# Optimization experiments

Hardware: AMD Instinct MI355X
Metric: run time of the kernel (lower is better)

The kernel has to match this reference:

```python
import jax, jax.numpy as jnp
import numpy as np

INPUT_DIM = 64
LATENT_DIM = 128
B, N = 16, 8192
SQRT3 = float(np.sqrt(3.0))
SQRT5 = float(np.sqrt(5.0))
PATH_COEFF = float(1.0 / np.sqrt(INPUT_DIM))  # e3nn 'element' path norm, w3j(0,l,l)=I/sqrt(2l+1)


def _spherical_harmonics_lmax2(pos):
    """e3nn o3.spherical_harmonics(lmax=2, normalize=True, normalization='component').
    Returns (sh0 [..],  sh1 [..,3], sh2 [..,5])."""
    n = pos * jax.lax.rsqrt(jnp.sum(pos * pos, axis=-1, keepdims=True))
    x, y, z = n[..., 0], n[..., 1], n[..., 2]
    sh0 = jnp.ones_like(x)
    sh1 = SQRT3 * n  # component norm: sqrt(3) * unit vector, order (x,y,z)
    # l=2 block (component norm = sqrt(5) * norm-normalized polynomials)
    sh2 = SQRT5 * jnp.stack([
        SQRT3 * x * z,
        SQRT3 * x * y,
        y * y - 0.5 * (x * x + z * z),
        SQRT3 * y * z,
        (SQRT3 / 2.0) * (z * z - x * x),
    ], axis=-1)
    return sh0, sh1, sh2


def setup_inputs() -> dict:
    key = jax.random.key(0)
    k1, k2, k3, k4 = jax.random.split(key, 4)
    features = jax.random.normal(k1, (B, N, INPUT_DIM), dtype=jnp.float32)
    pos = jax.random.normal(k2, (B, N, 3), dtype=jnp.float32)
    # e3nn FullyConnectedTensorProduct weights ~ N(0,1); one [u,w] matrix per path
    W0 = jax.random.normal(k3, (INPUT_DIM, LATENT_DIM), dtype=jnp.float32)  # 0e x 0e -> 0e
    W1 = jax.random.normal(k4, (INPUT_DIM, LATENT_DIM), dtype=jnp.float32)  # 0e x 1o -> 1o
    return {"features": features, "pos": pos, "W0": W0, "W1": W1}


def reference(features, pos, W0, W1):
    sh0, sh1, sh2 = _spherical_harmonics_lmax2(pos)  # sh2 has no output path (dropped)
    # scalar path: out[b,n,w] = coeff * sum_u feat[b,n,u] W0[u,w] * sh0
    scalars = PATH_COEFF * jnp.einsum('bnu,uw->bnw', features, W0) * sh0[..., None]
    # vector path: out[b,n,w,k] = coeff * (feat @ W1)[b,n,w] * sh1[b,n,k]
    vec = PATH_COEFF * jnp.einsum('bnu,uw->bnw', features, W1)
    vectors = vec[..., :, None] * sh1[..., None, :]  # [B,N,LATENT,3]
    latent = jnp.concatenate(
        [scalars, vectors.reshape(*vectors.shape[:-2], LATENT_DIM * 3)], axis=-1
    )  # [B, N, LATENT + 3*LATENT]
    return jnp.mean(latent, axis=1)  # [B, 4*LATENT]
```

## Files before the change

### kernel.cpp

```cpp
#include <hip/hip_runtime.h>

#define B_ 16
#define N_ 8192
#define U_ 64
#define W_ 128
#define BLOCKS_PER_B 32
#define ROWS_PER_BLOCK (N_ / BLOCKS_PER_B)
#define GRID_ (B_ * BLOCKS_PER_B)

typedef float f32x4 __attribute__((ext_vector_type(4)));


__global__ __launch_bounds__(256, 2) void so3_reduce_kernel(
    const float* __restrict__ feat,
    const float* __restrict__ pos,
    float* __restrict__ ws)
{
    const int blk   = blockIdx.x;
    const int b     = blk / BLOCKS_PER_B;
    const int chunk = blk % BLOCKS_PER_B;
    const int row0  = chunk * ROWS_PER_BLOCK;
    const int tid   = threadIdx.x;
    const int grp   = tid & 15;
    const int rsub  = tid >> 4;

    __shared__ f32x4 nlds[ROWS_PER_BLOCK];
    {
        const float* p = pos + ((size_t)b * N_ + row0 + tid) * 3;
        const float px = p[0], py = p[1], pz = p[2];
        const float inv = rsqrtf(px * px + py * py + pz * pz);
        f32x4 v;
        v.x = px * inv; v.y = py * inv; v.z = pz * inv; v.w = 1.0f;
        nlds[tid] = v;
    }
    __syncthreads();

    const f32x4* fbase = (const f32x4*)(feat + (size_t)b * N_ * U_);

    f32x4 fb[16];
    #pragma unroll
    for (int it = 0; it < 16; ++it) {
        const int nl = it * 16 + rsub;
        fb[it] = __builtin_nontemporal_load(
            &fbase[(size_t)(row0 + nl) * 16 + grp]);
    }

    float acc[4][4] = {{0.f,0.f,0.f,0.f},{0.f,0.f,0.f,0.f},
                       {0.f,0.f,0.f,0.f},{0.f,0.f,0.f,0.f}};

    #pragma unroll
    for (int it = 0; it < 16; ++it) {
        const int nl = it * 16 + rsub;
        const f32x4 f  = fb[it];
        const f32x4 nv = nlds[nl];
        #pragma unroll
        for (int k = 0; k < 4; ++k) {
            const float nk = (k == 0) ? nv.x : (k == 1) ? nv.y
                           : (k == 2) ? nv.z : nv.w;
            acc[0][k] = fmaf(f.x, nk, acc[0][k]);
            acc[1][k] = fmaf(f.y, nk, acc[1][k]);
            acc[2][k] = fmaf(f.z, nk, acc[2][k]);
            acc[3][k] = fmaf(f.w, nk, acc[3][k]);
        }
    }

    __shared__ float lds[256][17];
    #pragma unroll
    for (int i = 0; i < 4; ++i) {
        lds[tid][i * 4 + 0] = acc[i][0];
        lds[tid][i * 4 + 1] = acc[i][1];
        lds[tid][i * 4 + 2] = acc[i][2];
        lds[tid][i * 4 + 3] = acc[i][3];
    }
    __syncthreads();

    const int u    = tid >> 2;
    const int j    = tid & 3;
    const int ug   = u >> 2;
    const int sub  = u & 3;
    const int slot = (j == 0) ? (sub * 4 + 3) : (sub * 4 + (j - 1));
    float s = 0.f;
    #pragma unroll
    for (int src = 0; src < 16; ++src) {
        const int t = (src & 3) * 64 + (src >> 2) * 16 + ug;
        s += lds[t][slot];
    }
    ws[(size_t)blk * 256 + tid] = s;
}

__global__ __launch_bounds__(512) void so3_finalize_kernel(
    const float* __restrict__ ws,
    const float* __restrict__ W0,
    const float* __restrict__ W1,
    float* __restrict__ out)
{
    const int b   = blockIdx.x;
    const int tid = threadIdx.x;

    const int u4   = tid & 63;
    const int cgrp = tid >> 6;

    __shared__ float4 smf4[8][64];
    __shared__ float  sm[256];

    {
        const float4* base = (const float4*)(ws + (size_t)b * BLOCKS_PER_B * 256);
        float4 a = {0.f, 0.f, 0.f, 0.f};
        #pragma unroll
        for (int c = 0; c < 4; ++c) {
            const float4 v = base[(size_t)(cgrp * 4 + c) * 64 + u4];
            a.x += v.x; a.y += v.y; a.z += v.z; a.w += v.w;
        }
        smf4[cgrp][u4] = a;
    }
    __syncthreads();

    if (tid < 64) {
        float4 t = smf4[0][tid];
        #pragma unroll
        for (int g = 1; g < 8; ++g) {
            const float4 v = smf4[g][tid];
            t.x += v.x; t.y += v.y; t.z += v.z; t.w += v.w;
        }
        ((float4*)sm)[tid] = t;
    }
    __syncthreads();

    const float scaleS = 0.125f / (float)N_;
    const float scaleV = 0.125f * 1.7320508075688772f / (float)N_;

    const int o = tid;
    float acc = 0.f;
    if (o < 128) {
        #pragma unroll
        for (int uu = 0; uu < 64; ++uu) acc += sm[uu * 4] * W0[uu * 128 + o];
        out[b * 512 + o] = acc * scaleS;
    } else {
        const int idx = o - 128;
        const int w = idx / 3;
        const int k = idx - 3 * w;
        #pragma unroll
        for (int uu = 0; uu < 64; ++uu) acc += sm[uu * 4 + 1 + k] * W1[uu * 128 + w];
        out[b * 512 + 128 + idx] = acc * scaleV;
    }
}

extern "C" void kernel_launch(void* const* d_in, const int* in_sizes, int n_in,
                              void* d_out, int out_size, void* d_ws, size_t ws_size,
                              hipStream_t stream) {
    const float* feat = (const float*)d_in[0];
    const float* pos  = (const float*)d_in[1];
    const float* W0   = (const float*)d_in[2];
    const float* W1   = (const float*)d_in[3];
    float* out = (float*)d_out;
    float* ws  = (float*)d_ws;

    so3_reduce_kernel<<<GRID_, 256, 0, stream>>>(feat, pos, ws);
    so3_finalize_kernel<<<B_, 512, 0, stream>>>(ws, W0, W1, out);
}
```

Baseline: 12.90 us.

## Fuse reduce and finalize into one launch with flag-based inter-block handoff

```diff
diff --git a/kernel.cpp b/kernel.cpp
--- a/kernel.cpp
+++ b/kernel.cpp
@@ -6,142 +6,149 @@
 #define W_ 128
 #define BLOCKS_PER_B 32
 #define ROWS_PER_BLOCK (N_ / BLOCKS_PER_B)
-#define GRID_ (B_ * BLOCKS_PER_B)
+#define NPROD (B_ * BLOCKS_PER_B)
+#define NFIN  B_
+#define GRID_ (NPROD + NFIN)
+#define SENT 0x5AC3F00Du
 
 typedef float f32x4 __attribute__((ext_vector_type(4)));
 
 
-__global__ __launch_bounds__(256, 2) void so3_reduce_kernel(
+__global__ __launch_bounds__(256, 2) void so3_single_kernel(
     const float* __restrict__ feat,
     const float* __restrict__ pos,
+    const float* __restrict__ W0,
+    const float* __restrict__ W1,
+    float* __restrict__ out,
     float* __restrict__ ws)
 {
-    const int blk   = blockIdx.x;
-    const int b     = blk / BLOCKS_PER_B;
-    const int chunk = blk % BLOCKS_PER_B;
-    const int row0  = chunk * ROWS_PER_BLOCK;
-    const int tid   = threadIdx.x;
-    const int grp   = tid & 15;
-    const int rsub  = tid >> 4;
+    const int blk = blockIdx.x;
+    const int tid = threadIdx.x;
+    unsigned* flags = (unsigned*)(ws + (size_t)NPROD * 256);
 
-    __shared__ f32x4 nlds[ROWS_PER_BLOCK];
-    {
-        const float* p = pos + ((size_t)b * N_ + row0 + tid) * 3;
-        const float px = p[0], py = p[1], pz = p[2];
-        const float inv = rsqrtf(px * px + py * py + pz * pz);
-        f32x4 v;
-        v.x = px * inv; v.y = py * inv; v.z = pz * inv; v.w = 1.0f;
-        nlds[tid] = v;
+    if (blk < NPROD) {
+        const int b     = blk / BLOCKS_PER_B;
+        const int chunk = blk % BLOCKS_PER_B;
+        const int row0  = chunk * ROWS_PER_BLOCK;
+        const int grp   = tid & 15;
+        const int rsub  = tid >> 4;
+
+        __shared__ f32x4 nlds[ROWS_PER_BLOCK];
+        {
+            const float* p = pos + ((size_t)b * N_ + row0 + tid) * 3;
+            const float px = p[0], py = p[1], pz = p[2];
+            const float inv = rsqrtf(px * px + py * py + pz * pz);
+            f32x4 v;
+            v.x = px * inv; v.y = py * inv; v.z = pz * inv; v.w = 1.0f;
+            nlds[tid] = v;
+        }
+        __syncthreads();
+
+        const f32x4* fbase = (const f32x4*)(feat + (size_t)b * N_ * U_);
+
+        f32x4 fb[16];
+        #pragma unroll
+        for (int it = 0; it < 16; ++it) {
+            const int nl = it * 16 + rsub;
+            fb[it] = __builtin_nontemporal_load(
+                &fbase[(size_t)(row0 + nl) * 16 + grp]);
+        }
+
+        float acc[4][4] = {{0.f,0.f,0.f,0.f},{0.f,0.f,0.f,0.f},
+                           {0.f,0.f,0.f,0.f},{0.f,0.f,0.f,0.f}};
+
+        #pragma unroll
+        for (int it = 0; it < 16; ++it) {
+            const int nl = it * 16 + rsub;
+            const f32x4 f  = fb[it];
+            const f32x4 nv = nlds[nl];
+            #pragma unroll
+            for (int k = 0; k < 4; ++k) {
+                const float nk = (k == 0) ? nv.x : (k == 1) ? nv.y
+                               : (k == 2) ? nv.z : nv.w;
+                acc[0][k] = fmaf(f.x, nk, acc[0][k]);
+                acc[1][k] = fmaf(f.y, nk, acc[1][k]);
+                acc[2][k] = fmaf(f.z, nk, acc[2][k]);
+                acc[3][k] = fmaf(f.w, nk, acc[3][k]);
+            }
+        }
+
+        __shared__ float lds[256][17];
+        #pragma unroll
+        for (int i = 0; i < 4; ++i) {
+            lds[tid][i * 4 + 0] = acc[i][0];
+            lds[tid][i * 4 + 1] = acc[i][1];
+            lds[tid][i * 4 + 2] = acc[i][2];
+            lds[tid][i * 4 + 3] = acc[i][3];
+        }
+        __syncthreads();
+
+        const int u    = tid >> 2;
+        const int j    = tid & 3;
+        const int ug   = u >> 2;
+        const int sub  = u & 3;
+        const int slot = (j == 0) ? (sub * 4 + 3) : (sub * 4 + (j - 1));
+        float s = 0.f;
+        #pragma unroll
+        for (int src = 0; src < 16; ++src) {
+            const int t = (src & 3) * 64 + (src >> 2) * 16 + ug;
+            s += lds[t][slot];
+        }
+
+        (void)__hip_atomic_exchange(&ws[(size_t)blk * 256 + tid], s,
+                                    __ATOMIC_RELAXED, __HIP_MEMORY_SCOPE_AGENT);
+        asm volatile("s_waitcnt vmcnt(0)" ::: "memory");
+        __syncthreads();
+        if (tid == 0)
+            (void)__hip_atomic_exchange(&flags[blk], SENT,
+                                        __ATOMIC_RELAXED, __HIP_MEMORY_SCOPE_AGENT);
+        return;
+    }
+
+    const int b = blk - NPROD;
+
+    if (tid < BLOCKS_PER_B) {
+        while (__hip_atomic_load(&flags[b * BLOCKS_PER_B + tid],
+                                 __ATOMIC_RELAXED,
+                                 __HIP_MEMORY_SCOPE_AGENT) != SENT)
+            __builtin_amdgcn_s_sleep(1);
     }
     __syncthreads();
+    if (tid < BLOCKS_PER_B)
+        (void)__hip_atomic_exchange(&flags[b * BLOCKS_PER_B + tid], 0u,
+                                    __ATOMIC_RELAXED, __HIP_MEMORY_SCOPE_AGENT);
 
-    const f32x4* fbase = (const f32x4*)(feat + (size_t)b * N_ * U_);
-
-    f32x4 fb[16];
-    #pragma unroll
-    for (int it = 0; it < 16; ++it) {
-        const int nl = it * 16 + rsub;
-        fb[it] = __builtin_nontemporal_load(
-            &fbase[(size_t)(row0 + nl) * 16 + grp]);
+    float s = 0.f;
+    {
+        const float* base = ws + (size_t)b * BLOCKS_PER_B * 256;
+        #pragma unroll
+        for (int c = 0; c < BLOCKS_PER_B; ++c)
+            s += __hip_atomic_load(&base[(size_t)c * 256 + tid],
+                                   __ATOMIC_RELAXED, __HIP_MEMORY_SCOPE_AGENT);
     }
-
-    float acc[4][4] = {{0.f,0.f,0.f,0.f},{0.f,0.f,0.f,0.f},
-                       {0.f,0.f,0.f,0.f},{0.f,0.f,0.f,0.f}};
-
-    #pragma unroll
-    for (int it = 0; it < 16; ++it) {
-        const int nl = it * 16 + rsub;
-        const f32x4 f  = fb[it];
-        const f32x4 nv = nlds[nl];
-        #pragma unroll
-        for (int k = 0; k < 4; ++k) {
-            const float nk = (k == 0) ? nv.x : (k == 1) ? nv.y
-                           : (k == 2) ? nv.z : nv.w;
-            acc[0][k] = fmaf(f.x, nk, acc[0][k]);
-            acc[1][k] = fmaf(f.y, nk, acc[1][k]);
-            acc[2][k] = fmaf(f.z, nk, acc[2][k]);
-            acc[3][k] = fmaf(f.w, nk, acc[3][k]);
-        }
-    }
-
-    __shared__ float lds[256][17];
-    #pragma unroll
-    for (int i = 0; i < 4; ++i) {
-        lds[tid][i * 4 + 0] = acc[i][0];
-        lds[tid][i * 4 + 1] = acc[i][1];
-        lds[tid][i * 4 + 2] = acc[i][2];
-        lds[tid][i * 4 + 3] = acc[i][3];
-    }
-    __syncthreads();
-
-    const int u    = tid >> 2;
-    const int j    = tid & 3;
-    const int ug   = u >> 2;
-    const int sub  = u & 3;
-    const int slot = (j == 0) ? (sub * 4 + 3) : (sub * 4 + (j - 1));
-    float s = 0.f;
-    #pragma unroll
-    for (int src = 0; src < 16; ++src) {
-        const int t = (src & 3) * 64 + (src >> 2) * 16 + ug;
-        s += lds[t][slot];
-    }
-    ws[(size_t)blk * 256 + tid] = s;
-}
-
-__global__ __launch_bounds__(512) void so3_finalize_kernel(
-    const float* __restrict__ ws,
-    const float* __restrict__ W0,
-    const float* __restrict__ W1,
-    float* __restrict__ out)
-{
-    const int b   = blockIdx.x;
-    const int tid = threadIdx.x;
-
-    const int u4   = tid & 63;
-    const int cgrp = tid >> 6;
-
-    __shared__ float4 smf4[8][64];
-    __shared__ float  sm[256];
-
-    {
-        const float4* base = (const float4*)(ws + (size_t)b * BLOCKS_PER_B * 256);
-        float4 a = {0.f, 0.f, 0.f, 0.f};
-        #pragma unroll
-        for (int c = 0; c < 4; ++c) {
-            const float4 v = base[(size_t)(cgrp * 4 + c) * 64 + u4];
-            a.x += v.x; a.y += v.y; a.z += v.z; a.w += v.w;
-        }
-        smf4[cgrp][u4] = a;
-    }
-    __syncthreads();
-
-    if (tid < 64) {
-        float4 t = smf4[0][tid];
-        #pragma unroll
-        for (int g = 1; g < 8; ++g) {
-            const float4 v = smf4[g][tid];
-            t.x += v.x; t.y += v.y; t.z += v.z; t.w += v.w;
-        }
-        ((float4*)sm)[tid] = t;
-    }
+    __shared__ float sm[256];
+    sm[tid] = s;
     __syncthreads();
 
     const float scaleS = 0.125f / (float)N_;
     const float scaleV = 0.125f * 1.7320508075688772f / (float)N_;
 
-    const int o = tid;
-    float acc = 0.f;
-    if (o < 128) {
-        #pragma unroll
-        for (int uu = 0; uu < 64; ++uu) acc += sm[uu * 4] * W0[uu * 128 + o];
-        out[b * 512 + o] = acc * scaleS;
-    } else {
-        const int idx = o - 128;
-        const int w = idx / 3;
-        const int k = idx - 3 * w;
-        #pragma unroll
-        for (int uu = 0; uu < 64; ++uu) acc += sm[uu * 4 + 1 + k] * W1[uu * 128 + w];
-        out[b * 512 + 128 + idx] = acc * scaleV;
+    #pragma unroll
+    for (int half = 0; half < 2; ++half) {
+        const int o = tid + half * 256;
+        float acc = 0.f;
+        if (o < 128) {
+            #pragma unroll
+            for (int u = 0; u < 64; ++u) acc += sm[u * 4 + 0] * W0[u * 128 + o];
+            out[b * 512 + o] = acc * scaleS;
+        } else {
+            const int idx = o - 128;
+            const int w = idx / 3;
+            const int k = idx - 3 * w;
+            #pragma unroll
+            for (int u = 0; u < 64; ++u) acc += sm[u * 4 + 1 + k] * W1[u * 128 + w];
+            out[b * 512 + 128 + idx] = acc * scaleV;
+        }
     }
 }
 
@@ -155,6 +162,5 @@
     float* out = (float*)d_out;
     float* ws  = (float*)d_ws;
 
-    so3_reduce_kernel<<<GRID_, 256, 0, stream>>>(feat, pos, ws);
-    so3_finalize_kernel<<<B_, 512, 0, stream>>>(ws, W0, W1, out);
+    so3_single_kernel<<<GRID_, 256, 0, stream>>>(feat, pos, W0, W1, out, ws);
 }
```

Result: no change. 12.67 us (-1.8%).
